# Performance work log

Hardware: AMD Instinct MI355X
Metric: run time of the kernel (lower is better)

The kernel has to match this reference:

```python
import jax, jax.numpy as jnp
import numpy as np

N, E, D, ED = 50000, 500000, 128, 10
EPS = 1e-5


def _glorot(key, shape):
    return jax.random.normal(key, shape, jnp.float32) / np.sqrt(shape[0]).astype(np.float32)


def setup_inputs() -> dict:
    key = jax.random.key(0)
    ks = jax.random.split(key, 8)
    x = jax.random.normal(ks[0], (N, D), jnp.float32)
    edge_index = jax.random.randint(ks[1], (2, E), 0, N, jnp.int32)
    edge_attr = jax.random.normal(ks[2], (E, ED), jnp.float32)
    # edge encoder: Linear(edge_dim -> F_in)
    W_ee = _glorot(ks[3], (ED, D)); b_ee = jnp.zeros((D,), jnp.float32)
    # pre MLP (pre_layers=1): Linear(3*F_in -> F_in) on cat([x_i, x_j, e])
    W_pre = _glorot(ks[4], (3 * D, D)); b_pre = jnp.zeros((D,), jnp.float32)
    # post MLP (post_layers=1): Linear((4 aggr * 3 scalers + 1)*F_in -> F_out)
    W_post = _glorot(ks[5], (13 * D, D)); b_post = jnp.zeros((D,), jnp.float32)
    # final lin: Linear(towers*F_out -> out_channels)
    W_lin = _glorot(ks[6], (D, D)); b_lin = jnp.zeros((D,), jnp.float32)
    return {"x": x, "edge_attr": edge_attr, "W_ee": W_ee, "b_ee": b_ee,
            "W_pre": W_pre, "b_pre": b_pre, "W_post": W_post, "b_post": b_post,
            "W_lin": W_lin, "b_lin": b_lin, "edge_index": edge_index}


def reference(x, edge_attr, W_ee, b_ee, W_pre, b_pre, W_post, b_post, W_lin, b_lin, edge_index):
    n = x.shape[0]
    src, dst = edge_index[0], edge_index[1]  # x_j = x[src], x_i = x[dst]

    # --- message: pre-MLP over cat([x_i, x_j, edge_enc]) ---
    ea = edge_attr @ W_ee + b_ee                                   # [E, D]
    h = jnp.concatenate([x[dst], x[src], ea], axis=-1)             # [E, 3D]
    m = h @ W_pre + b_pre                                          # [E, D]

    # --- multi-aggregation at target nodes: mean / max / min / std ---
    cnt = jax.ops.segment_sum(jnp.ones((m.shape[0],), x.dtype), dst, num_segments=n)  # [N]
    deg = jnp.maximum(cnt, 1.0)[:, None]                           # clamp(1), [N,1]
    has_edge = (cnt > 0)[:, None]
    mean = jax.ops.segment_sum(m, dst, num_segments=n) / deg
    mean_sq = jax.ops.segment_sum(m * m, dst, num_segments=n) / deg
    std = jnp.sqrt(jax.nn.relu(mean_sq - mean * mean) + EPS)
    mx = jnp.where(has_edge, jax.ops.segment_max(m, dst, num_segments=n), 0.0)
    mn = jnp.where(has_edge, jax.ops.segment_min(m, dst, num_segments=n), 0.0)
    agg = jnp.concatenate([mean, mx, mn, std], axis=-1)            # [N, 4D]

    # --- degree scalers: identity / amplification / attenuation ---
    avg_log = jnp.mean(jnp.log(cnt + 1.0))                         # avg_deg['log']
    s_log = jnp.log(deg + 1.0)                                     # [N,1]
    scaled = jnp.concatenate([agg, agg * (s_log / avg_log), agg * (avg_log / s_log)], axis=-1)  # [N,12D]

    # --- post MLP on cat([x, aggregated]) then final linear ---
    out = jnp.concatenate([x, scaled], axis=-1) @ W_post + b_post  # [N, D]
    return out @ W_lin + b_lin
```

## Files before the change

kernel.cpp:

```cpp
#include <hip/hip_runtime.h>
#include <hip/hip_bf16.h>
#include <float.h>
#include <math.h>

#define N_NODES 50000
#define N_EDGES 500000
#define D 128
#define ED 10
#define EPS_PNA 1e-5f
#define SCAN_NTILES 49
#define XGEMM_BLOCKS 391
#define HIST_BLOCKS 1954

typedef __hip_bfloat16 bf16;
typedef unsigned short ushort;
typedef unsigned int uint;
typedef __attribute__((ext_vector_type(8))) short short8;
typedef __attribute__((ext_vector_type(4))) float f32x4;

__device__ __forceinline__ ushort f2bf(float f) {
    __hip_bfloat16 h = __float2bfloat16(f);
    return *reinterpret_cast<ushort*>(&h);
}
__device__ __forceinline__ float bf2f(ushort u) {
    return __uint_as_float(((uint)u) << 16);
}

__global__ __launch_bounds__(256) void k_scanA(const int* __restrict__ cnt,
                                               int* __restrict__ bsum,
                                               float* __restrict__ blog) {
    const int t = threadIdx.x;
    const int base = blockIdx.x * 1024;
    int s = 0; float ls = 0.f;
    #pragma unroll
    for (int k = 0; k < 4; ++k) {
        const int idx = base + t + k * 256;
        if (idx < N_NODES) {
            const int c = cnt[idx];
            s += c;
            ls += logf((float)c + 1.0f);
        }
    }
    #pragma unroll
    for (int off = 32; off > 0; off >>= 1) {
        s += __shfl_down(s, off, 64);
        ls += __shfl_down(ls, off, 64);
    }
    __shared__ int ws[4]; __shared__ float wl[4];
    const int wv = t >> 6, l = t & 63;
    if (l == 0) { ws[wv] = s; wl[wv] = ls; }
    __syncthreads();
    if (t == 0) {
        bsum[blockIdx.x] = ws[0] + ws[1] + ws[2] + ws[3];
        blog[blockIdx.x] = wl[0] + wl[1] + wl[2] + wl[3];
    }
}

__global__ __launch_bounds__(256) void k_scanC(const int* __restrict__ cnt,
                                               const int* __restrict__ bsum,
                                               const float* __restrict__ blog,
                                               int* __restrict__ rowstart,
                                               int* __restrict__ cursor,
                                               float* __restrict__ avglog) {
    const int t = threadIdx.x, lane = t & 63, wv = t >> 6;
    __shared__ int sboff;
    if (t < 64) {
        const int v = (t < SCAN_NTILES) ? bsum[t] : 0;
        int s = v;
        #pragma unroll
        for (int off = 1; off < 64; off <<= 1) {
            const int u = __shfl_up(s, off, 64);
            if (t >= off) s += u;
        }
        if (t == blockIdx.x) sboff = s - v;
        if (blockIdx.x == 0 && t == SCAN_NTILES - 1)
            rowstart[N_NODES] = s;
        if (blockIdx.x == 0) {
            float lg = (t < SCAN_NTILES) ? blog[t] : 0.f;
            #pragma unroll
            for (int off = 32; off > 0; off >>= 1) lg += __shfl_down(lg, off, 64);
            if (t == 0) avglog[0] = lg * (1.0f / (float)N_NODES);
        }
    }
    const int base = blockIdx.x * 1024;
    int c[4]; int ts = 0;
    #pragma unroll
    for (int k = 0; k < 4; ++k) {
        const int idx = base + t * 4 + k;
        c[k] = (idx < N_NODES) ? cnt[idx] : 0;
        ts += c[k];
    }
    int s = ts;
    #pragma unroll
    for (int off = 1; off < 64; off <<= 1) {
        const int u = __shfl_up(s, off, 64);
        if (lane >= off) s += u;
    }
    __shared__ int wtot[4], woff[4];
    if (lane == 63) wtot[wv] = s;
    __syncthreads();
    if (t == 0) {
        int r = 0;
        #pragma unroll
        for (int i = 0; i < 4; ++i) { woff[i] = r; r += wtot[i]; }
    }
    __syncthreads();
    int excl = sboff + woff[wv] + (s - ts);
    #pragma unroll
    for (int k = 0; k < 4; ++k) {
        const int idx = base + t * 4 + k;
        if (idx < N_NODES) { rowstart[idx] = excl; cursor[idx] = excl; }
        excl += c[k];
    }
}

__global__ void k_scatter(const int* __restrict__ ei, const float* __restrict__ eattr,
                          int* __restrict__ cursor, uint4* __restrict__ csr_rec) {
    int e = blockIdx.x * blockDim.x + threadIdx.x;
    if (e < N_EDGES) {
        const int dst = ei[N_EDGES + e];
        const int src = ei[e];
        const float2* ea2 = (const float2*)(eattr + (size_t)e * ED);
        const float2 a0 = ea2[0], a1 = ea2[1], a2 = ea2[2], a3 = ea2[3], a4 = ea2[4];
        const int pos = atomicAdd(&cursor[dst], 1);
        uint4* o = csr_rec + (size_t)pos * 3;
        o[0] = make_uint4(__float_as_uint(a0.x), __float_as_uint(a0.y),
                          __float_as_uint(a1.x), __float_as_uint(a1.y));
        o[1] = make_uint4(__float_as_uint(a2.x), __float_as_uint(a2.y),
                          __float_as_uint(a3.x), __float_as_uint(a3.y));
        o[2] = make_uint4(__float_as_uint(a4.x), __float_as_uint(a4.y), (uint)src, 0u);
    }
}

__global__ __launch_bounds__(256) void k_wprep(
    const float* __restrict__ Wee, const float* __restrict__ bee,
    const float* __restrict__ Wpre, const float* __restrict__ bpre,
    const float* __restrict__ Wpost, const float* __restrict__ bpost,
    const float* __restrict__ Wlin, const float* __restrict__ blin,
    float* __restrict__ W4, float* __restrict__ bp,
    ushort* __restrict__ WxT,
    ushort* __restrict__ WaT,
    float* __restrict__ b_comb,
    int* __restrict__ cnt)
{
    __shared__ float smem[128 * 128];
    const int t = threadIdx.x;
    const int bx = blockIdx.x;

    if (bx < 104) {
        float* Wl = smem;
        for (int i = t; i < 128 * 128 / 4; i += 256)
            ((float4*)Wl)[i] = ((const float4*)Wlin)[i];
        __syncthreads();
        const int j = t & 127, rp = t >> 7;
        const int kr0 = bx * 16 + rp * 8;
        for (int r = 0; r < 8; ++r) {
            const int kr = kr0 + r;
            const float* wrow = Wpost + (size_t)kr * 128;
            float acc = 0.f;
            #pragma unroll 8
            for (int m = 0; m < 128; ++m) acc += wrow[m] * Wl[m * 128 + j];
            const ushort v = f2bf(acc);
            if (kr < 128)       WxT[(256 + j) * 128 + kr] = v;
            else if (kr < 640)  WaT[(size_t)j * 512 + (kr - 128)] = v;
            else if (kr < 1152) WaT[(size_t)(128 + j) * 512 + (kr - 640)] = v;
            else                WaT[(size_t)(256 + j) * 512 + (kr - 1152)] = v;
        }
        if (bx == 0 && t < 128) {
            float acc = 0.f;
            #pragma unroll 8
            for (int m = 0; m < 128; ++m) acc += bpost[m] * Wl[m * 128 + t];
            b_comb[t] = acc + blin[t];
        }
    } else if (bx == 104) {
        float* wee_s = smem;
        float* bee_s = smem + ED * D;
        for (int i = t; i < ED * D; i += 256) wee_s[i] = Wee[i];
        if (t < 128) bee_s[t] = bee[t];
        __syncthreads();
        if (t < 128) {
            float acc[ED];
            #pragma unroll
            for (int r = 0; r < ED; ++r) acc[r] = 0.f;
            float bacc = 0.f;
            for (int k = 0; k < D; ++k) {
                const float w3 = Wpre[(size_t)(2 * D + k) * D + t];
                #pragma unroll
                for (int r = 0; r < ED; ++r) acc[r] += wee_s[r * D + k] * w3;
                bacc += bee_s[k] * w3;
            }
            #pragma unroll
            for (int r = 0; r < ED; ++r) W4[r * D + t] = acc[r];
            bp[t] = bpre[t] + bacc;
        }
    } else if (bx < 121) {
        const int slice = (bx < 113) ? 0 : 1;
        const int id = (bx - (slice ? 113 : 105)) * 256 + t;
        const float* src = Wpre + (size_t)slice * 128 * 128;
        ushort* dst = WxT + (size_t)slice * 128 * 128;
        const int col = id & 127;
        const int k0 = (id >> 7) * 8;
        ushort tmp[8];
        #pragma unroll
        for (int r = 0; r < 8; ++r) tmp[r] = f2bf(src[(size_t)(k0 + r) * 128 + col]);
        *(uint4*)(dst + (size_t)col * 128 + k0) = *(uint4*)tmp;
    } else {
        const int i = (bx - 121) * 256 + t;
        if (i < N_NODES) cnt[i] = 0;
    }
}

__global__ __launch_bounds__(256) void k_hx(
    const int* __restrict__ ei, int* __restrict__ cnt,
    const float* __restrict__ x, const ushort* __restrict__ WxT,
    const float* __restrict__ b_comb,
    ushort* __restrict__ Y1b, ushort* __restrict__ Y2b, float* __restrict__ out)
{
    const int t = threadIdx.x;
    if (blockIdx.x >= XGEMM_BLOCKS) {
        const int e = (blockIdx.x - XGEMM_BLOCKS) * 256 + t;
        if (e < N_EDGES) atomicAdd(&cnt[ei[N_EDGES + e]], 1);
        return;
    }

    __shared__ __align__(16) ushort Alds[128 * 136];
    __shared__ __align__(16) ushort Hlds[128 * 136];
    const int nb = blockIdx.x * 128;

    #pragma unroll
    for (int g = 0; g < 8; ++g) {
        const int idx = t + g * 256;
        const int row = idx >> 4, kk = (idx & 15) * 8;
        const int node = nb + row;
        uint4 v = make_uint4(0u, 0u, 0u, 0u);
        if (node < N_NODES) {
            const float4 f0 = *(const float4*)(x + (size_t)node * 128 + kk);
            const float4 f1 = *(const float4*)(x + (size_t)node * 128 + kk + 4);
            __hip_bfloat162 p0 = __float22bfloat162_rn(make_float2(f0.x, f0.y));
            __hip_bfloat162 p1 = __float22bfloat162_rn(make_float2(f0.z, f0.w));
            __hip_bfloat162 p2 = __float22bfloat162_rn(make_float2(f1.x, f1.y));
            __hip_bfloat162 p3 = __float22bfloat162_rn(make_float2(f1.z, f1.w));
            v.x = *(uint*)&p0; v.y = *(uint*)&p1; v.z = *(uint*)&p2; v.w = *(uint*)&p3;
        }
        *(uint4*)&Hlds[row * 136 + kk] = v;
    }

    const int w = t >> 6, l = t & 63;
    const int wr = w >> 1, wc = w & 1;
    const int quad = l >> 4, lr = l & 15;

    for (int sy = 0; sy < 3; ++sy) {
        __syncthreads();
        #pragma unroll
        for (int g = 0; g < 8; ++g) {
            const int idx = t + g * 256;
            const int row = idx >> 4, kk = (idx & 15) * 8;
            *(uint4*)&Alds[row * 136 + kk] =
                *(const uint4*)(WxT + ((size_t)sy * 128 + row) * 128 + kk);
        }
        __syncthreads();

        f32x4 acc[4][4];
        #pragma unroll
        for (int i = 0; i < 4; ++i)
            #pragma unroll
            for (int j = 0; j < 4; ++j) acc[i][j] = (f32x4){0.f, 0.f, 0.f, 0.f};

        #pragma unroll
        for (int s = 0; s < 4; ++s) {
            short8 av[4], bv[4];
            #pragma unroll
            for (int i = 0; i < 4; ++i)
                av[i] = *(const short8*)&Alds[(wr * 64 + i * 16 + lr) * 136 + s * 32 + quad * 8];
            #pragma unroll
            for (int j = 0; j < 4; ++j)
                bv[j] = *(const short8*)&Hlds[(wc * 64 + j * 16 + lr) * 136 + s * 32 + quad * 8];
            #pragma unroll
            for (int i = 0; i < 4; ++i)
                #pragma unroll
                for (int j = 0; j < 4; ++j)
                    acc[i][j] = __builtin_amdgcn_mfma_f32_16x16x32_bf16(av[i], bv[j], acc[i][j], 0, 0, 0);
        }

        #pragma unroll
        for (int i = 0; i < 4; ++i) {
            const int col = wr * 64 + i * 16 + quad * 4;
            #pragma unroll
            for (int j = 0; j < 4; ++j) {
                const int node = nb + wc * 64 + j * 16 + lr;
                if (node < N_NODES) {
                    const f32x4 v = acc[i][j];
                    if (sy == 2) {
                        *(float4*)(out + (size_t)node * 128 + col) =
                            make_float4(v.x + b_comb[col],     v.y + b_comb[col + 1],
                                        v.z + b_comb[col + 2], v.w + b_comb[col + 3]);
                    } else {
                        ushort* dst = (sy == 0) ? Y1b : Y2b;
                        ushort pk[4];
                        pk[0] = f2bf(v.x); pk[1] = f2bf(v.y);
                        pk[2] = f2bf(v.z); pk[3] = f2bf(v.w);
                        *(uint2*)(dst + (size_t)node * 128 + col) = *(uint2*)pk;
                    }
                }
            }
        }
    }
}

__global__ __launch_bounds__(256) void k_pull(
    const uint4* __restrict__ csr_rec, const float* __restrict__ W4,
    const float* __restrict__ bp, const ushort* __restrict__ Y1b,
    const ushort* __restrict__ Y2b,
    const int* __restrict__ rowstart,
    ushort* __restrict__ aggB)
{
    __shared__ float2 w4s[ED][64];
    const int t = threadIdx.x;
    for (int i = t; i < ED * 64; i += 256)
        w4s[i >> 6][i & 63] = ((const float2*)W4)[i];
    __syncthreads();

    const int wv = t >> 6, l = t & 63;
    const int n = blockIdx.x * 4 + wv;
    const int r0 = __builtin_amdgcn_readfirstlane(rowstart[n]);
    const int r1 = __builtin_amdgcn_readfirstlane(rowstart[n + 1]);
    const int d = r1 - r0;

    float s0 = 0.f, s1 = 0.f, ss0 = 0.f, ss1 = 0.f;
    float mx0 = -FLT_MAX, mx1 = -FLT_MAX, mn0 = FLT_MAX, mn1 = FLT_MAX;
    const __hip_bfloat162* Y2p = (const __hip_bfloat162*)Y2b;

    uint4 ra, rb, rc;
    if (d > 0) {
        const uint4* rp = csr_rec + (size_t)r0 * 3;
        ra = rp[0]; rb = rp[1]; rc = rp[2];
    }
    for (int i = r0; i < r1; ++i) {
        const int inext = (i + 1 < r1) ? (i + 1) : i;
        const uint4* rp = csr_rec + (size_t)inext * 3;
        const uint4 na = rp[0], nb4 = rp[1], nc = rp[2];

        const int src = (int)rc.z;
        const float2 y2 = __bfloat1622float2(Y2p[(size_t)src * 64 + l]);

        float ea[10];
        ea[0] = __uint_as_float(ra.x); ea[1] = __uint_as_float(ra.y);
        ea[2] = __uint_as_float(ra.z); ea[3] = __uint_as_float(ra.w);
        ea[4] = __uint_as_float(rb.x); ea[5] = __uint_as_float(rb.y);
        ea[6] = __uint_as_float(rb.z); ea[7] = __uint_as_float(rb.w);
        ea[8] = __uint_as_float(rc.x); ea[9] = __uint_as_float(rc.y);

        float q0 = 0.f, q1 = 0.f;
        #pragma unroll
        for (int r = 0; r < ED; ++r) {
            const float2 wv2 = w4s[r][l];
            q0 += ea[r] * wv2.x;
            q1 += ea[r] * wv2.y;
        }
        const float z0 = y2.x + q0, z1 = y2.y + q1;
        s0 += z0; s1 += z1;
        ss0 += z0 * z0; ss1 += z1 * z1;
        mx0 = fmaxf(mx0, z0); mx1 = fmaxf(mx1, z1);
        mn0 = fminf(mn0, z0); mn1 = fminf(mn1, z1);

        ra = na; rb = nb4; rc = nc;
    }

    const float2 bpw = ((const float2*)bp)[l];
    const float2 y1 = __bfloat1622float2(((const __hip_bfloat162*)Y1b)[(size_t)n * 64 + l]);
    float mean0, mean1, vmx0, vmx1, vmn0, vmn1, st0, st1;
    if (d > 0) {
        const float inv = 1.f / (float)d;
        const float mz0 = s0 * inv, mz1 = s1 * inv;
        const float c0 = y1.x + bpw.x, c1 = y1.y + bpw.y;
        mean0 = mz0 + c0; mean1 = mz1 + c1;
        st0 = sqrtf(fmaxf(ss0 * inv - mz0 * mz0, 0.f) + EPS_PNA);
        st1 = sqrtf(fmaxf(ss1 * inv - mz1 * mz1, 0.f) + EPS_PNA);
        vmx0 = mx0 + c0; vmx1 = mx1 + c1;
        vmn0 = mn0 + c0; vmn1 = mn1 + c1;
    } else {
        mean0 = mean1 = 0.f;
        vmx0 = vmx1 = vmn0 = vmn1 = 0.f;
        st0 = st1 = sqrtf(EPS_PNA);
    }
    __hip_bfloat162* aggv = (__hip_bfloat162*)aggB;
    const size_t b0 = (size_t)n * 256;
    aggv[b0 + l]       = __float22bfloat162_rn(make_float2(mean0, mean1));
    aggv[b0 + 64 + l]  = __float22bfloat162_rn(make_float2(vmx0, vmx1));
    aggv[b0 + 128 + l] = __float22bfloat162_rn(make_float2(vmn0, vmn1));
    aggv[b0 + 192 + l] = __float22bfloat162_rn(make_float2(st0, st1));
}

__global__ __launch_bounds__(256) void k_agg(
    const ushort* __restrict__ aggB,
    const ushort* __restrict__ WaT,
    const int* __restrict__ cnt, const float* __restrict__ avglog,
    float* __restrict__ out)
{
    __shared__ __align__(16) ushort Alds[128 * 72];
    __shared__ __align__(16) ushort Hlds[64 * 72];
    __shared__ float r1s[64], r2s[64];

    const int t = threadIdx.x;
    const int nb = blockIdx.x * 64;
    if (t < 64) {
        const int node = nb + t;
        float deg = 1.f;
        if (node < N_NODES) deg = fmaxf((float)cnt[node], 1.f);
        const float sl = logf(deg + 1.f);
        const float al = avglog[0];
        r1s[t] = sl / al;
        r2s[t] = al / sl;
    }

    const int w = t >> 6, l = t & 63;
    const int wr = w >> 1, wc = w & 1;
    const int quad = l >> 4, lr = l & 15;

    f32x4 comb[4][2];
    #pragma unroll
    for (int i = 0; i < 4; ++i)
        #pragma unroll
        for (int j = 0; j < 2; ++j) comb[i][j] = (f32x4){0.f, 0.f, 0.f, 0.f};

    #define STAGE_A(SL)                                                           \
        _Pragma("unroll")                                                         \
        for (int g = 0; g < 4; ++g) {                                             \
            const int idx = t + g * 256;                                          \
            const int row = idx >> 3, kk = (idx & 7) * 8;                         \
            *(uint4*)&Alds[row * 72 + kk] =                                       \
                *(const uint4*)(WaT + ((size_t)((SL) * 128 + row)) * 512 + k0 + kk); \
        }

    #define MFMA_EPOCH(SL)                                                        \
        {                                                                         \
            f32x4 acc[4][2];                                                      \
            _Pragma("unroll")                                                     \
            for (int i = 0; i < 4; ++i)                                           \
                _Pragma("unroll")                                                 \
                for (int j = 0; j < 2; ++j) acc[i][j] = (f32x4){0.f,0.f,0.f,0.f}; \
            _Pragma("unroll")                                                     \
            for (int s = 0; s < 2; ++s) {                                         \
                short8 av[4], bv[2];                                              \
                _Pragma("unroll")                                                 \
                for (int i = 0; i < 4; ++i)                                       \
                    av[i] = *(const short8*)&Alds[(wr*64 + i*16 + lr)*72 + s*32 + quad*8]; \
                _Pragma("unroll")                                                 \
                for (int j = 0; j < 2; ++j)                                       \
                    bv[j] = *(const short8*)&Hlds[(wc*32 + j*16 + lr)*72 + s*32 + quad*8]; \
                _Pragma("unroll")                                                 \
                for (int i = 0; i < 4; ++i)                                       \
                    _Pragma("unroll")                                             \
                    for (int j = 0; j < 2; ++j)                                   \
                        acc[i][j] = __builtin_amdgcn_mfma_f32_16x16x32_bf16(av[i], bv[j], acc[i][j], 0, 0, 0); \
            }                                                                     \
            _Pragma("unroll")                                                     \
            for (int j = 0; j < 2; ++j) {                                         \
                const int nl = wc * 32 + j * 16 + lr;                             \
                const float r = ((SL) == 0) ? 1.f : ((SL) == 1) ? r1s[nl] : r2s[nl]; \
                _Pragma("unroll")                                                 \
                for (int i = 0; i < 4; ++i) {                                     \
                    comb[i][j].x += r * acc[i][j].x;                              \
                    comb[i][j].y += r * acc[i][j].y;                              \
                    comb[i][j].z += r * acc[i][j].z;                              \
                    comb[i][j].w += r * acc[i][j].w;                              \
                }                                                                 \
            }                                                                     \
        }

    for (int kc = 0; kc < 8; ++kc) {
        const int k0 = kc * 64;
        __syncthreads();
        #pragma unroll
        for (int g = 0; g < 2; ++g) {
            const int idx = t + g * 256;
            const int row = idx >> 3, kk = (idx & 7) * 8;
            const int node = nb + row;
            uint4 v = make_uint4(0u, 0u, 0u, 0u);
            if (node < N_NODES)
                v = *(const uint4*)(aggB + (size_t)node * 512 + k0 + kk);
            *(uint4*)&Hlds[row * 72 + kk] = v;
        }
        STAGE_A(0);
        __syncthreads();
        MFMA_EPOCH(0);
        __syncthreads();
        STAGE_A(1);
        __syncthreads();
        MFMA_EPOCH(1);
        __syncthreads();
        STAGE_A(2);
        __syncthreads();
        MFMA_EPOCH(2);
    }
    #undef STAGE_A
    #undef MFMA_EPOCH

    #pragma unroll
    for (int i = 0; i < 4; ++i) {
        const int col = wr * 64 + i * 16 + quad * 4;
        #pragma unroll
        for (int j = 0; j < 2; ++j) {
            const int node = nb + wc * 32 + j * 16 + lr;
            if (node < N_NODES) {
                float* op = out + (size_t)node * 128 + col;
                const float4 cur = *(const float4*)op;
                const f32x4 v = comb[i][j];
                *(float4*)op = make_float4(cur.x + v.x, cur.y + v.y,
                                           cur.z + v.z, cur.w + v.w);
            }
        }
    }
}

extern "C" void kernel_launch(void* const* d_in, const int* in_sizes, int n_in,
                              void* d_out, int out_size, void* d_ws, size_t ws_size,
                              hipStream_t stream) {
    const float* x     = (const float*)d_in[0];
    const float* eattr = (const float*)d_in[1];
    const float* Wee   = (const float*)d_in[2];
    const float* bee   = (const float*)d_in[3];
    const float* Wpre  = (const float*)d_in[4];
    const float* bpre  = (const float*)d_in[5];
    const float* Wpost = (const float*)d_in[6];
    const float* bpost = (const float*)d_in[7];
    const float* Wlin  = (const float*)d_in[8];
    const float* blin  = (const float*)d_in[9];
    const int*   ei    = (const int*)d_in[10];
    float* out = (float*)d_out;

    ushort* aggB = (ushort*)d_ws;
    ushort* Y1b  = aggB + (size_t)N_NODES * 512;
    ushort* Y2b  = Y1b  + (size_t)N_NODES * 128;
    ushort* WxT  = Y2b  + (size_t)N_NODES * 128;
    ushort* WaT  = WxT + 384 * 128;
    float*  W4   = (float*)(WaT + 384 * 512);
    float*  bp   = W4 + ED * D;
    float*  b_comb = bp + D;
    float*  avglog = b_comb + D;
    int*   cnt      = (int*)(avglog + 4);
    int*   rowstart = cnt + N_NODES;
    int*   cursor   = rowstart + N_NODES + 4;
    uint4* csr_rec  = (uint4*)(cursor + N_NODES);
    int*   bsum     = (int*)(csr_rec + (size_t)N_EDGES * 3);
    float* blog     = (float*)(bsum + 64);

    k_wprep<<<317, 256, 0, stream>>>(Wee, bee, Wpre, bpre, Wpost, bpost, Wlin, blin,
                                     W4, bp, WxT, WaT, b_comb, cnt);
    k_hx<<<XGEMM_BLOCKS + HIST_BLOCKS, 256, 0, stream>>>(ei, cnt, x, WxT, b_comb,
                                                         Y1b, Y2b, out);
    k_scanA<<<SCAN_NTILES, 256, 0, stream>>>(cnt, bsum, blog);
    k_scanC<<<SCAN_NTILES, 256, 0, stream>>>(cnt, bsum, blog, rowstart, cursor, avglog);
    k_scatter<<<(N_EDGES + 255) / 256, 256, 0, stream>>>(ei, eattr, cursor, csr_rec);
    k_pull<<<N_NODES / 4, 256, 0, stream>>>(csr_rec, W4, bp, Y1b, Y2b,
                                            rowstart, aggB);
    k_agg<<<(N_NODES + 63) / 64, 256, 0, stream>>>(aggB, WaT, cnt, avglog, out);
}
```

Baseline: 300.4 us.

## Stage all three scaler weight slices at once and defer scaling to epilogue

The aggregation GEMM kernel now loads all three degree-scaler weight slices into separate LDS buffers in one go and keeps three sets of accumulators across the whole K loop. The per-node scale factors are applied once in the epilogue instead of after every k-chunk. This cuts the barriers per k-chunk from six to two and removes the per-epoch scale-and-add work. In exchange, LDS use roughly triples, to about 64KB, and accumulator registers triple, to 96 floats per thread, which may lower occupancy.

```diff
diff --git a/kernel.cpp b/kernel.cpp
--- a/kernel.cpp
+++ b/kernel.cpp
@@ -397,7 +397,7 @@
     const int* __restrict__ cnt, const float* __restrict__ avglog,
     float* __restrict__ out)
 {
-    __shared__ __align__(16) ushort Alds[128 * 72];
+    __shared__ __align__(16) ushort Alds[3][128 * 72];
     __shared__ __align__(16) ushort Hlds[64 * 72];
     __shared__ float r1s[64], r2s[64];
 
@@ -417,56 +417,13 @@
     const int wr = w >> 1, wc = w & 1;
     const int quad = l >> 4, lr = l & 15;
 
-    f32x4 comb[4][2];
-    #pragma unroll
-    for (int i = 0; i < 4; ++i)
-        #pragma unroll
-        for (int j = 0; j < 2; ++j) comb[i][j] = (f32x4){0.f, 0.f, 0.f, 0.f};
-
-    #define STAGE_A(SL)                                                           \
-        _Pragma("unroll")                                                         \
-        for (int g = 0; g < 4; ++g) {                                             \
-            const int idx = t + g * 256;                                          \
-            const int row = idx >> 3, kk = (idx & 7) * 8;                         \
-            *(uint4*)&Alds[row * 72 + kk] =                                       \
-                *(const uint4*)(WaT + ((size_t)((SL) * 128 + row)) * 512 + k0 + kk); \
-        }
-
-    #define MFMA_EPOCH(SL)                                                        \
-        {                                                                         \
-            f32x4 acc[4][2];                                                      \
-            _Pragma("unroll")                                                     \
-            for (int i = 0; i < 4; ++i)                                           \
-                _Pragma("unroll")                                                 \
-                for (int j = 0; j < 2; ++j) acc[i][j] = (f32x4){0.f,0.f,0.f,0.f}; \
-            _Pragma("unroll")                                                     \
-            for (int s = 0; s < 2; ++s) {                                         \
-                short8 av[4], bv[2];                                              \
-                _Pragma("unroll")                                                 \
-                for (int i = 0; i < 4; ++i)                                       \
-                    av[i] = *(const short8*)&Alds[(wr*64 + i*16 + lr)*72 + s*32 + quad*8]; \
-                _Pragma("unroll")                                                 \
-                for (int j = 0; j < 2; ++j)                                       \
-                    bv[j] = *(const short8*)&Hlds[(wc*32 + j*16 + lr)*72 + s*32 + quad*8]; \
-                _Pragma("unroll")                                                 \
-                for (int i = 0; i < 4; ++i)                                       \
-                    _Pragma("unroll")                                             \
-                    for (int j = 0; j < 2; ++j)                                   \
-                        acc[i][j] = __builtin_amdgcn_mfma_f32_16x16x32_bf16(av[i], bv[j], acc[i][j], 0, 0, 0); \
-            }                                                                     \
-            _Pragma("unroll")                                                     \
-            for (int j = 0; j < 2; ++j) {                                         \
-                const int nl = wc * 32 + j * 16 + lr;                             \
-                const float r = ((SL) == 0) ? 1.f : ((SL) == 1) ? r1s[nl] : r2s[nl]; \
-                _Pragma("unroll")                                                 \
-                for (int i = 0; i < 4; ++i) {                                     \
-                    comb[i][j].x += r * acc[i][j].x;                              \
-                    comb[i][j].y += r * acc[i][j].y;                              \
-                    comb[i][j].z += r * acc[i][j].z;                              \
-                    comb[i][j].w += r * acc[i][j].w;                              \
-                }                                                                 \
-            }                                                                     \
-        }
+    f32x4 acc[3][4][2];
+    #pragma unroll
+    for (int sl = 0; sl < 3; ++sl)
+        #pragma unroll
+        for (int i = 0; i < 4; ++i)
+            #pragma unroll
+            for (int j = 0; j < 2; ++j) acc[sl][i][j] = (f32x4){0.f, 0.f, 0.f, 0.f};
 
     for (int kc = 0; kc < 8; ++kc) {
         const int k0 = kc * 64;
@@ -481,20 +438,36 @@
                 v = *(const uint4*)(aggB + (size_t)node * 512 + k0 + kk);
             *(uint4*)&Hlds[row * 72 + kk] = v;
         }
-        STAGE_A(0);
+        #pragma unroll
+        for (int sl = 0; sl < 3; ++sl) {
+            #pragma unroll
+            for (int g = 0; g < 4; ++g) {
+                const int idx = t + g * 256;
+                const int row = idx >> 3, kk = (idx & 7) * 8;
+                *(uint4*)&Alds[sl][row * 72 + kk] =
+                    *(const uint4*)(WaT + ((size_t)(sl * 128 + row)) * 512 + k0 + kk);
+            }
+        }
         __syncthreads();
-        MFMA_EPOCH(0);
-        __syncthreads();
-        STAGE_A(1);
-        __syncthreads();
-        MFMA_EPOCH(1);
-        __syncthreads();
-        STAGE_A(2);
-        __syncthreads();
-        MFMA_EPOCH(2);
-    }
-    #undef STAGE_A
-    #undef MFMA_EPOCH
+        #pragma unroll
+        for (int sl = 0; sl < 3; ++sl) {
+            #pragma unroll
+            for (int s = 0; s < 2; ++s) {
+                short8 av[4], bv[2];
+                #pragma unroll
+                for (int i = 0; i < 4; ++i)
+                    av[i] = *(const short8*)&Alds[sl][(wr * 64 + i * 16 + lr) * 72 + s * 32 + quad * 8];
+                #pragma unroll
+                for (int j = 0; j < 2; ++j)
+                    bv[j] = *(const short8*)&Hlds[(wc * 32 + j * 16 + lr) * 72 + s * 32 + quad * 8];
+                #pragma unroll
+                for (int i = 0; i < 4; ++i)
+                    #pragma unroll
+                    for (int j = 0; j < 2; ++j)
+                        acc[sl][i][j] = __builtin_amdgcn_mfma_f32_16x16x32_bf16(av[i], bv[j], acc[sl][i][j], 0, 0, 0);
+            }
+        }
+    }
 
     #pragma unroll
     for (int i = 0; i < 4; ++i) {
@@ -503,11 +476,18 @@
         for (int j = 0; j < 2; ++j) {
             const int node = nb + wc * 32 + j * 16 + lr;
             if (node < N_NODES) {
+                const int nl = wc * 32 + j * 16 + lr;
+                const float r1 = r1s[nl], r2 = r2s[nl];
                 float* op = out + (size_t)node * 128 + col;
                 const float4 cur = *(const float4*)op;
-                const f32x4 v = comb[i][j];
-                *(float4*)op = make_float4(cur.x + v.x, cur.y + v.y,
-                                           cur.z + v.z, cur.w + v.w);
+                const f32x4 a0 = acc[0][i][j];
+                const f32x4 a1 = acc[1][i][j];
+                const f32x4 a2 = acc[2][i][j];
+                *(float4*)op = make_float4(
+                    cur.x + a0.x + r1 * a1.x + r2 * a2.x,
+                    cur.y + a0.y + r1 * a1.y + r2 * a2.y,
+                    cur.z + a0.z + r1 * a1.z + r2 * a2.z,
+                    cur.w + a0.w + r1 * a1.w + r2 * a2.w);
             }
         }
     }
```

Result: faster. 293.9 us (-2.2%).
